# Optimization experiments

Measured on AMD Instinct MI355X. Metric: run time of the kernel, lower is better.

## Reference

```python
import jax, jax.numpy as jnp
import numpy as np

N = 8192        # num_nodes (also num output classes per the module)
F_IN = 512      # num_features
H = 64          # gcn_dim
E = N * 64      # edges (avg_degree 64)


def setup_inputs() -> dict:
    key = jax.random.key(0)
    k_x, k_e, k_w1, k_w2 = jax.random.split(key, 4)
    x = jax.random.normal(k_x, (N, F_IN), dtype=jnp.float32)
    edge_index = jax.random.randint(k_e, (2, E), 0, N, dtype=jnp.int64)
    # Glorot-ish init for the two GCN layer weights
    W1 = jax.random.normal(k_w1, (F_IN, H), dtype=jnp.float32) * (1.0 / np.sqrt(F_IN))
    b1 = jnp.zeros((H,), dtype=jnp.float32)
    W2 = jax.random.normal(k_w2, (H, N), dtype=jnp.float32) * (1.0 / np.sqrt(H))
    b2 = jnp.zeros((N,), dtype=jnp.float32)
    return {"x": x, "edge_index": edge_index, "W1": W1, "b1": b1, "W2": W2, "b2": b2}


def _gcn_conv(x, edge_index, W, b):
    """GCNConv: out = D^{-1/2} (A + I) D^{-1/2} (x @ W) + b."""
    n = x.shape[0]
    loops = jnp.arange(n, dtype=edge_index.dtype)
    src = jnp.concatenate([edge_index[0], loops])  # message source nodes
    dst = jnp.concatenate([edge_index[1], loops])  # aggregation targets
    deg = jax.ops.segment_sum(jnp.ones_like(dst, dtype=x.dtype), dst, num_segments=n)
    dinv = jnp.where(deg > 0, jax.lax.rsqrt(deg), 0.0)
    norm = dinv[src] * dinv[dst]                   # [E+n]
    xw = x @ W                                     # transform first (smaller msgs when W shrinks dim)
    msgs = xw[src] * norm[:, None]                 # gather + scale
    return jax.ops.segment_sum(msgs, dst, num_segments=n) + b


def reference(x, edge_index, W1, b1, W2, b2):
    h = jax.nn.relu(_gcn_conv(x, edge_index, W1, b1))   # [N, H]
    logits = _gcn_conv(h, edge_index, W2, b2)           # [N, N]
    return jax.nn.log_softmax(logits, axis=1)
```

## Files before the change

### kernel.cpp

```cpp
#include <hip/hip_runtime.h>
#include <hip/hip_bf16.h>

typedef __attribute__((ext_vector_type(8))) short short8;
typedef __attribute__((ext_vector_type(16))) float f32x16;

#define NN 8192
#define FIN 512
#define HD 64
#define LOG2E 1.44269504088896f

#if __has_builtin(__builtin_amdgcn_exp2f)
#define EXP2(x) __builtin_amdgcn_exp2f(x)
#else
#define EXP2(x) exp2f(x)
#endif

__global__ void k_pack_zero(const float* __restrict__ W2, __hip_bfloat16* __restrict__ w2p,
                            int* __restrict__ cnt) {
    int i = blockIdx.x * blockDim.x + threadIdx.x;
    if (i < NN) cnt[i] = 0;
    int k  = i >> 13;
    int cc = i & 8191;
    int c32 = cc >> 5, cl = cc & 31;
    int kc = k >> 4, hh = (k >> 3) & 1, j = k & 7;
    int dsti = ((c32 * 4 + kc) * 64 + hh * 32 + cl) * 8 + j;
    w2p[dsti] = __float2bfloat16(W2[i]);
}

__global__ void k_count(const int* __restrict__ dst, int E, int* __restrict__ cnt) {
    int e = blockIdx.x * blockDim.x + threadIdx.x;
    if (e < E) atomicAdd(&cnt[dst[e]], 1);
}

__global__ __launch_bounds__(1024) void k_scan(const int* __restrict__ cnt,
        int* __restrict__ offs, int* __restrict__ cursor, float* __restrict__ dinv) {
    __shared__ int wsh[16];
    int t = threadIdx.x;
    int lane = t & 63, wv = t >> 6;
    int v[8], loc[8];
    int s = 0;
#pragma unroll
    for (int j = 0; j < 8; ++j) { v[j] = cnt[t*8+j]; loc[j] = s; s += v[j]; }
    int inc = s;
#pragma unroll
    for (int d = 1; d < 64; d <<= 1) {
        int up = __shfl_up(inc, d, 64);
        if (lane >= d) inc += up;
    }
    if (lane == 63) wsh[wv] = inc;
    __syncthreads();
    if (t < 16) {
        int mv = wsh[t];
        int winc = mv;
#pragma unroll
        for (int d = 1; d < 16; d <<= 1) {
            int up = __shfl_up(winc, d, 16);
            if (t >= d) winc += up;
        }
        wsh[t] = winc - mv;
    }
    __syncthreads();
    int base = wsh[wv] + (inc - s);
#pragma unroll
    for (int j = 0; j < 8; ++j) {
        int o = base + loc[j];
        offs[t*8+j]   = o;
        cursor[t*8+j] = o;
        dinv[t*8+j]   = rsqrtf((float)(v[j] + 1));
    }
    if (t == 1023) offs[NN] = base + s;
}

__global__ void k_scatter(const int* __restrict__ src, const int* __restrict__ dst, int E,
        int* __restrict__ cursor, int* __restrict__ ssrc) {
    int e = blockIdx.x * blockDim.x + threadIdx.x;
    if (e < E) {
        int pos = atomicAdd(&cursor[dst[e]], 1);
        ssrc[pos] = src[e];
    }
}

__global__ __launch_bounds__(256) void k_gemm1(const float* __restrict__ x,
        const float* __restrict__ W1, const float* __restrict__ dinv,
        float* __restrict__ xws) {
    __shared__ float Xs[16][132];
    int t = threadIdx.x;
    int c  = t & 63;
    int rg = t >> 6;
    int br = blockIdx.x * 16;
    float acc[4] = {0.f, 0.f, 0.f, 0.f};
    for (int k0 = 0; k0 < FIN; k0 += 128) {
        __syncthreads();
        int row_ld = t >> 4, kcol = (t & 15) * 8;
        const float* xp = x + (br + row_ld) * FIN + k0 + kcol;
        float4 v0 = *(const float4*)xp;
        float4 v1 = *(const float4*)(xp + 4);
        *(float4*)&Xs[row_ld][kcol]     = v0;
        *(float4*)&Xs[row_ld][kcol + 4] = v1;
        __syncthreads();
#pragma unroll 8
        for (int kk = 0; kk < 128; ++kk) {
            float w = W1[(k0 + kk) * HD + c];
#pragma unroll
            for (int r = 0; r < 4; ++r)
                acc[r] += Xs[rg*4 + r][kk] * w;
        }
    }
#pragma unroll
    for (int r = 0; r < 4; ++r) {
        int row = br + rg*4 + r;
        xws[row * HD + c] = acc[r] * dinv[row];
    }
}

__global__ __launch_bounds__(256) void k_agg1(const float* __restrict__ xws,
        const int* __restrict__ offs, const int* __restrict__ ssrc,
        const float* __restrict__ dinv, const float* __restrict__ b1,
        float* __restrict__ hs) {
    int lane = threadIdx.x & 63;
    int node = (blockIdx.x << 2) + (threadIdx.x >> 6);
    const float* xp = xws + lane;
    float acc = xp[node * HD];
    int beg = offs[node], end = offs[node + 1];
    for (int base = beg; base < end; base += 64) {
        int rem = end - base;
        int n = rem < 64 ? rem : 64;
        int idx = (lane < n) ? ssrc[base + lane] : 0;
        int j = 0;
        for (; j + 8 <= n; j += 8) {
            int s0 = __shfl(idx, j+0, 64), s1 = __shfl(idx, j+1, 64);
            int s2 = __shfl(idx, j+2, 64), s3 = __shfl(idx, j+3, 64);
            int s4 = __shfl(idx, j+4, 64), s5 = __shfl(idx, j+5, 64);
            int s6 = __shfl(idx, j+6, 64), s7 = __shfl(idx, j+7, 64);
            float v0 = xp[s0*HD], v1 = xp[s1*HD], v2 = xp[s2*HD], v3 = xp[s3*HD];
            float v4 = xp[s4*HD], v5 = xp[s5*HD], v6 = xp[s6*HD], v7 = xp[s7*HD];
            acc += ((v0+v1)+(v2+v3)) + ((v4+v5)+(v6+v7));
        }
        for (; j < n; ++j) {
            int s = __shfl(idx, j, 64);
            acc += xp[s*HD];
        }
    }
    float dv = dinv[node];
    float h = fmaxf(acc * dv + b1[lane], 0.f);
    hs[node * HD + lane] = h * dv;
}

__global__ __launch_bounds__(256) void k_agg2(const float* __restrict__ hs,
        const int* __restrict__ offs, const int* __restrict__ ssrc,
        const float* __restrict__ dinv, __hip_bfloat16* __restrict__ gbf) {
    int lane = threadIdx.x & 63;
    int node = (blockIdx.x << 2) + (threadIdx.x >> 6);
    const float* hp = hs + lane;
    float acc = hp[node * HD];
    int beg = offs[node], end = offs[node + 1];
    for (int base = beg; base < end; base += 64) {
        int rem = end - base;
        int n = rem < 64 ? rem : 64;
        int idx = (lane < n) ? ssrc[base + lane] : 0;
        int j = 0;
        for (; j + 8 <= n; j += 8) {
            int s0 = __shfl(idx, j+0, 64), s1 = __shfl(idx, j+1, 64);
            int s2 = __shfl(idx, j+2, 64), s3 = __shfl(idx, j+3, 64);
            int s4 = __shfl(idx, j+4, 64), s5 = __shfl(idx, j+5, 64);
            int s6 = __shfl(idx, j+6, 64), s7 = __shfl(idx, j+7, 64);
            float v0 = hp[s0*HD], v1 = hp[s1*HD], v2 = hp[s2*HD], v3 = hp[s3*HD];
            float v4 = hp[s4*HD], v5 = hp[s5*HD], v6 = hp[s6*HD], v7 = hp[s7*HD];
            acc += ((v0+v1)+(v2+v3)) + ((v4+v5)+(v6+v7));
        }
        for (; j < n; ++j) {
            int s = __shfl(idx, j, 64);
            acc += hp[s*HD];
        }
    }
    gbf[node * HD + lane] = __float2bfloat16(acc * dinv[node]);
}

__global__ __launch_bounds__(512) void k_fused(
        const __hip_bfloat16* __restrict__ gbf,
        const __hip_bfloat16* __restrict__ w2p,
        const float* __restrict__ b2,
        float* __restrict__ out) {
    __shared__ float red[32][8];
    __shared__ float Lsh[32];
    const unsigned short* g  = (const unsigned short*)gbf;
    const unsigned short* wp = (const unsigned short*)w2p;
    int t = threadIdx.x;
    int lane = t & 63, wv = t >> 6;
    int cl = lane & 31, hh = lane >> 5;
    int row0 = blockIdx.x * 32;

    short8 a[4];
#pragma unroll
    for (int kc = 0; kc < 4; ++kc)
        a[kc] = *(const short8*)(g + (row0 + cl) * HD + kc*16 + hh*8);

    float sm[16];
#pragma unroll
    for (int r = 0; r < 16; ++r) sm[r] = 0.f;

    for (int it = 0; it < 32; ++it) {
        int c32 = wv * 32 + it;
        const unsigned short* bp = wp + c32 * 2048 + lane * 8;
        float bias = b2[c32 * 32 + cl];
        f32x16 d;
#pragma unroll
        for (int r = 0; r < 16; ++r) d[r] = 0.f;
#pragma unroll
        for (int kc = 0; kc < 4; ++kc) {
            short8 b = *(const short8*)(bp + kc * 512);
            d = __builtin_amdgcn_mfma_f32_32x32x16_bf16(a[kc], b, d, 0, 0, 0);
        }
#pragma unroll
        for (int r = 0; r < 16; ++r)
            sm[r] += EXP2((d[r] + bias) * LOG2E);
    }
#pragma unroll
    for (int r = 0; r < 16; ++r) {
#pragma unroll
        for (int msk = 1; msk < 32; msk <<= 1)
            sm[r] += __shfl_xor(sm[r], msk, 64);
    }
    if (cl == 0) {
#pragma unroll
        for (int r = 0; r < 16; ++r)
            red[(r & 3) + 8 * (r >> 2) + 4 * hh][wv] = sm[r];
    }
    __syncthreads();
    if (t < 32) {
        float s = 0.f;
#pragma unroll
        for (int j = 0; j < 8; ++j) s += red[t][j];
        Lsh[t] = logf(s);
    }
    __syncthreads();
    float L[16];
#pragma unroll
    for (int r = 0; r < 16; ++r)
        L[r] = Lsh[(r & 3) + 8 * (r >> 2) + 4 * hh];

    for (int it = 0; it < 32; ++it) {
        int c32 = wv * 32 + it;
        const unsigned short* bp = wp + c32 * 2048 + lane * 8;
        float bias = b2[c32 * 32 + cl];
        f32x16 d;
#pragma unroll
        for (int r = 0; r < 16; ++r) d[r] = 0.f;
#pragma unroll
        for (int kc = 0; kc < 4; ++kc) {
            short8 b = *(const short8*)(bp + kc * 512);
            d = __builtin_amdgcn_mfma_f32_32x32x16_bf16(a[kc], b, d, 0, 0, 0);
        }
        float* op = out + (size_t)row0 * NN + c32 * 32 + cl;
#pragma unroll
        for (int r = 0; r < 16; ++r) {
            int rp = (r & 3) + 8 * (r >> 2) + 4 * hh;
            __builtin_nontemporal_store(d[r] + bias - L[r], op + (size_t)rp * NN);
        }
    }
}

extern "C" void kernel_launch(void* const* d_in, const int* in_sizes, int n_in,
                              void* d_out, int out_size, void* d_ws, size_t ws_size,
                              hipStream_t stream) {
    const float* x  = (const float*)d_in[0];
    const int*   ei = (const int*)d_in[1];
    const float* W1 = (const float*)d_in[2];
    const float* b1 = (const float*)d_in[3];
    const float* W2 = (const float*)d_in[4];
    const float* b2 = (const float*)d_in[5];
    float* out = (float*)d_out;
    int E = in_sizes[1] / 2;
    const int* esrc = ei;
    const int* edst = ei + E;

    char* w = (char*)d_ws;
    int*   cnt    = (int*)(w);
    int*   offs   = (int*)(w + (32 << 10));
    int*   cursor = (int*)(w + (68 << 10));
    float* dinv   = (float*)(w + (100 << 10));
    __hip_bfloat16* gbf = (__hip_bfloat16*)(w + (192 << 10));
    __hip_bfloat16* w2p = (__hip_bfloat16*)(w + (192 << 10) + (1 << 20));

    size_t total = (size_t)NN * NN;
    float* hs   = out + total - (size_t)NN * HD;
    float* xws  = hs  - (size_t)NN * HD;
    int*   ssrc = (int*)xws - E;

    int eb = (E + 255) / 256;
    k_pack_zero<<<(HD * NN) / 256, 256, 0, stream>>>(W2, w2p, cnt);
    k_count  <<<eb, 256, 0, stream>>>(edst, E, cnt);
    k_scan   <<<1, 1024, 0, stream>>>(cnt, offs, cursor, dinv);
    k_scatter<<<eb, 256, 0, stream>>>(esrc, edst, E, cursor, ssrc);
    k_gemm1  <<<NN / 16, 256, 0, stream>>>(x, W1, dinv, xws);
    k_agg1   <<<NN / 4, 256, 0, stream>>>(xws, offs, ssrc, dinv, b1, hs);
    k_agg2   <<<NN / 4, 256, 0, stream>>>(hs, offs, ssrc, dinv, gbf);
    k_fused  <<<NN / 32, 512, 0, stream>>>(gbf, w2p, b2, out);
}
```

Before: 451.5 us.

## Fuse second-layer aggregation into final GEMM/log-softmax kernel and vectorize gemm1 LDS reads

```diff
diff --git a/kernel.cpp b/kernel.cpp
--- a/kernel.cpp
+++ b/kernel.cpp
@@ -3,6 +3,7 @@
 
 typedef __attribute__((ext_vector_type(8))) short short8;
 typedef __attribute__((ext_vector_type(16))) float f32x16;
+typedef __attribute__((ext_vector_type(4))) float f32x4;
 
 #define NN 8192
 #define FIN 512
@@ -83,7 +84,7 @@
 __global__ __launch_bounds__(256) void k_gemm1(const float* __restrict__ x,
         const float* __restrict__ W1, const float* __restrict__ dinv,
         float* __restrict__ xws) {
-    __shared__ float Xs[16][132];
+    __shared__ alignas(16) float Xs[16][132];
     int t = threadIdx.x;
     int c  = t & 63;
     int rg = t >> 6;
@@ -98,12 +99,21 @@
         *(float4*)&Xs[row_ld][kcol]     = v0;
         *(float4*)&Xs[row_ld][kcol + 4] = v1;
         __syncthreads();
-#pragma unroll 8
-        for (int kk = 0; kk < 128; ++kk) {
-            float w = W1[(k0 + kk) * HD + c];
-#pragma unroll
-            for (int r = 0; r < 4; ++r)
-                acc[r] += Xs[rg*4 + r][kk] * w;
+        int rg4 = rg * 4;
+#pragma unroll 4
+        for (int kk = 0; kk < 128; kk += 4) {
+            f32x4 x0 = *(const f32x4*)&Xs[rg4 + 0][kk];
+            f32x4 x1 = *(const f32x4*)&Xs[rg4 + 1][kk];
+            f32x4 x2 = *(const f32x4*)&Xs[rg4 + 2][kk];
+            f32x4 x3 = *(const f32x4*)&Xs[rg4 + 3][kk];
+#pragma unroll
+            for (int q = 0; q < 4; ++q) {
+                float w = W1[(k0 + kk + q) * HD + c];
+                acc[0] += x0[q] * w;
+                acc[1] += x1[q] * w;
+                acc[2] += x2[q] * w;
+                acc[3] += x3[q] * w;
+            }
         }
     }
 #pragma unroll
@@ -260,6 +270,137 @@
     }
 }
 
+__global__ __launch_bounds__(512) void k_fused2(
+        const float* __restrict__ hs,
+        const int* __restrict__ offs, const int* __restrict__ ssrc,
+        const float* __restrict__ dinv,
+        const __hip_bfloat16* __restrict__ w2p,
+        const float* __restrict__ b2,
+        float* __restrict__ out) {
+    __shared__ alignas(16) unsigned short gsh[32][72];
+    __shared__ float red[32][8];
+    __shared__ float Lsh[32];
+    const unsigned short* wp = (const unsigned short*)w2p;
+    int t = threadIdx.x;
+    int lane = t & 63, wv = t >> 6;
+    int cl = lane & 31, hh = lane >> 5;
+    int row0 = blockIdx.x * 32;
+
+    const float* hp = hs + lane;
+    for (int q = 0; q < 4; ++q) {
+        int r = wv * 4 + q;
+        int node = row0 + r;
+        float acc = hp[node * HD];
+        int beg = offs[node], end = offs[node + 1];
+        for (int base = beg; base < end; base += 64) {
+            int rem = end - base;
+            int n = rem < 64 ? rem : 64;
+            int idx = (lane < n) ? ssrc[base + lane] : 0;
+            int j = 0;
+            for (; j + 8 <= n; j += 8) {
+                int s0 = __shfl(idx, j+0, 64), s1 = __shfl(idx, j+1, 64);
+                int s2 = __shfl(idx, j+2, 64), s3 = __shfl(idx, j+3, 64);
+                int s4 = __shfl(idx, j+4, 64), s5 = __shfl(idx, j+5, 64);
+                int s6 = __shfl(idx, j+6, 64), s7 = __shfl(idx, j+7, 64);
+                float v0 = hp[s0*HD], v1 = hp[s1*HD], v2 = hp[s2*HD], v3 = hp[s3*HD];
+                float v4 = hp[s4*HD], v5 = hp[s5*HD], v6 = hp[s6*HD], v7 = hp[s7*HD];
+                acc += ((v0+v1)+(v2+v3)) + ((v4+v5)+(v6+v7));
+            }
+            for (; j < n; ++j) {
+                int s = __shfl(idx, j, 64);
+                acc += hp[s*HD];
+            }
+        }
+        __hip_bfloat16 hv = __float2bfloat16(acc * dinv[node]);
+        gsh[r][lane] = *reinterpret_cast<unsigned short*>(&hv);
+    }
+    __syncthreads();
+
+    short8 a[4];
+#pragma unroll
+    for (int kc = 0; kc < 4; ++kc)
+        a[kc] = *(const short8*)&gsh[cl][kc * 16 + hh * 8];
+
+    const unsigned short* bpw = wp + (wv * 32) * 2048 + lane * 8;
+    const float* bias_c = b2 + wv * 1024 + cl;
+
+    float sm[16];
+#pragma unroll
+    for (int r = 0; r < 16; ++r) sm[r] = 0.f;
+
+    short8 bc[4];
+#pragma unroll
+    for (int kc = 0; kc < 4; ++kc) bc[kc] = *(const short8*)(bpw + kc * 512);
+    for (int it = 0; it < 32; ++it) {
+        int itn = (it + 1) & 31;
+        const unsigned short* bq = bpw + itn * 2048;
+        short8 bn[4];
+#pragma unroll
+        for (int kc = 0; kc < 4; ++kc) bn[kc] = *(const short8*)(bq + kc * 512);
+        float bias = bias_c[it * 32];
+        f32x16 d;
+#pragma unroll
+        for (int r = 0; r < 16; ++r) d[r] = 0.f;
+#pragma unroll
+        for (int kc = 0; kc < 4; ++kc)
+            d = __builtin_amdgcn_mfma_f32_32x32x16_bf16(a[kc], bc[kc], d, 0, 0, 0);
+#pragma unroll
+        for (int r = 0; r < 16; ++r)
+            sm[r] += EXP2((d[r] + bias) * LOG2E);
+#pragma unroll
+        for (int kc = 0; kc < 4; ++kc) bc[kc] = bn[kc];
+    }
+#pragma unroll
+    for (int r = 0; r < 16; ++r) {
+#pragma unroll
+        for (int msk = 1; msk < 32; msk <<= 1)
+            sm[r] += __shfl_xor(sm[r], msk, 64);
+    }
+    if (cl == 0) {
+#pragma unroll
+        for (int r = 0; r < 16; ++r)
+            red[(r & 3) + 8 * (r >> 2) + 4 * hh][wv] = sm[r];
+    }
+    __syncthreads();
+    if (t < 32) {
+        float s = 0.f;
+#pragma unroll
+        for (int j = 0; j < 8; ++j) s += red[t][j];
+        Lsh[t] = logf(s);
+    }
+    __syncthreads();
+    float L[16];
+#pragma unroll
+    for (int r = 0; r < 16; ++r)
+        L[r] = Lsh[(r & 3) + 8 * (r >> 2) + 4 * hh];
+
+#pragma unroll
+    for (int kc = 0; kc < 4; ++kc) bc[kc] = *(const short8*)(bpw + kc * 512);
+    for (int it = 0; it < 32; ++it) {
+        int itn = (it + 1) & 31;
+        const unsigned short* bq = bpw + itn * 2048;
+        short8 bn[4];
+#pragma unroll
+        for (int kc = 0; kc < 4; ++kc) bn[kc] = *(const short8*)(bq + kc * 512);
+        int c32 = wv * 32 + it;
+        float bias = bias_c[it * 32];
+        f32x16 d;
+#pragma unroll
+        for (int r = 0; r < 16; ++r) d[r] = 0.f;
+#pragma unroll
+        for (int kc = 0; kc < 4; ++kc)
+            d = __builtin_amdgcn_mfma_f32_32x32x16_bf16(a[kc], bc[kc], d, 0, 0, 0);
+        float* op = out + (size_t)row0 * NN + c32 * 32 + cl;
+#pragma unroll
+        for (int r = 0; r < 16; ++r) {
+            int rp = (r & 3) + 8 * (r >> 2) + 4 * hh;
+            __builtin_nontemporal_store(d[r] + bias - L[r], op + (size_t)rp * NN);
+        }
+#pragma unroll
+        for (int kc = 0; kc < 4; ++kc) bc[kc] = bn[kc];
+    }
+}
+
 extern "C" void kernel_launch(void* const* d_in, const int* in_sizes, int n_in,
                               void* d_out, int out_size, void* d_ws, size_t ws_size,
                               hipStream_t stream) {
@@ -279,21 +420,34 @@
     int*   offs   = (int*)(w + (32 << 10));
     int*   cursor = (int*)(w + (68 << 10));
     float* dinv   = (float*)(w + (100 << 10));
-    __hip_bfloat16* gbf = (__hip_bfloat16*)(w + (192 << 10));
-    __hip_bfloat16* w2p = (__hip_bfloat16*)(w + (192 << 10) + (1 << 20));
+    __hip_bfloat16* w2p = (__hip_bfloat16*)(w + (192 << 10));
 
     size_t total = (size_t)NN * NN;
-    float* hs   = out + total - (size_t)NN * HD;
-    float* xws  = hs  - (size_t)NN * HD;
-    int*   ssrc = (int*)xws - E;
+    size_t need_fused = (size_t)(192 << 10) + (1 << 20) + (size_t)NN * HD * sizeof(float);
+    bool fused_path = ws_size >= need_fused;
 
     int eb = (E + 255) / 256;
     k_pack_zero<<<(HD * NN) / 256, 256, 0, stream>>>(W2, w2p, cnt);
     k_count  <<<eb, 256, 0, stream>>>(edst, E, cnt);
     k_scan   <<<1, 1024, 0, stream>>>(cnt, offs, cursor, dinv);
-    k_scatter<<<eb, 256, 0, stream>>>(esrc, edst, E, cursor, ssrc);
-    k_gemm1  <<<NN / 16, 256, 0, stream>>>(x, W1, dinv, xws);
-    k_agg1   <<<NN / 4, 256, 0, stream>>>(xws, offs, ssrc, dinv, b1, hs);
-    k_agg2   <<<NN / 4, 256, 0, stream>>>(hs, offs, ssrc, dinv, gbf);
-    k_fused  <<<NN / 32, 512, 0, stream>>>(gbf, w2p, b2, out);
-}
+
+    if (fused_path) {
+        float* hs   = (float*)(w + (192 << 10) + (1 << 20));
+        float* xws  = out + total - (size_t)NN * HD;
+        int*   ssrc = (int*)xws - E;
+        k_scatter<<<eb, 256, 0, stream>>>(esrc, edst, E, cursor, ssrc);
+        k_gemm1  <<<NN / 16, 256, 0, stream>>>(x, W1, dinv, xws);
+        k_agg1   <<<NN / 4, 256, 0, stream>>>(xws, offs, ssrc, dinv, b1, hs);
+        k_fused2 <<<NN / 32, 512, 0, stream>>>(hs, offs, ssrc, dinv, w2p, b2, out);
+    } else {
+        __hip_bfloat16* gbf = (__hip_bfloat16*)(w + (192 << 10) + (1 << 20));
+        float* hs   = out + total - (size_t)NN * HD;
+        float* xws  = hs  - (size_t)NN * HD;
+        int*   ssrc = (int*)xws - E;
+        k_scatter<<<eb, 256, 0, stream>>>(esrc, edst, E, cursor, ssrc);
+        k_gemm1  <<<NN / 16, 256, 0, stream>>>(x, W1, dinv, xws);
+        k_agg1   <<<NN / 4, 256, 0, stream>>>(xws, offs, ssrc, dinv, b1, hs);
+        k_agg2   <<<NN / 4, 256, 0, stream>>>(hs, offs, ssrc, dinv, gbf);
+        k_fused  <<<NN / 32, 512, 0, stream>>>(gbf, w2p, b2, out);
+    }
+}
```

After: 437.7 us. -3.1%, faster.
